# Performance work log

Measured on AMD Instinct MI355X. Metric: run time of the kernel, lower is better.

## Reference

```python
import jax, jax.numpy as jnp
import numpy as np

LAYER_NUM = 2
NUM_CLS = 128
HIDDEN = 256
NUM_NODES = 1024


def setup_inputs() -> dict:
    key = jax.random.key(0)
    ks = jax.random.split(key, 12)
    s = 0.05
    return {
        "x": jax.random.normal(ks[0], (NUM_NODES, HIDDEN), jnp.float32),
        "knowledge": jax.random.uniform(ks[1], (NUM_CLS, NUM_CLS), jnp.float32) / NUM_CLS,
        "w3w": jax.random.normal(ks[2], (HIDDEN, 2 * HIDDEN), jnp.float32) * s,
        "b3w": jax.random.normal(ks[3], (HIDDEN,), jnp.float32) * s,
        "u3": jax.random.normal(ks[4], (HIDDEN, HIDDEN), jnp.float32) * s,
        "bu3": jax.random.normal(ks[5], (HIDDEN,), jnp.float32) * s,
        "w4w": jax.random.normal(ks[6], (HIDDEN, 2 * HIDDEN), jnp.float32) * s,
        "b4w": jax.random.normal(ks[7], (HIDDEN,), jnp.float32) * s,
        "w5w": jax.random.normal(ks[8], (HIDDEN, 2 * HIDDEN), jnp.float32) * s,
        "b5w": jax.random.normal(ks[9], (HIDDEN,), jnp.float32) * s,
        "u5": jax.random.normal(ks[10], (HIDDEN, HIDDEN), jnp.float32) * s,
        "bu5": jax.random.normal(ks[11], (HIDDEN,), jnp.float32) * s,
    }


def reference(x, knowledge, w3w, b3w, u3, bu3, w4w, b4w, w5w, b5w, u5, bu5):
    N, H = x.shape
    C = knowledge.shape[0]
    # hidden[n, c, :] = x[n, :]  (repeat per class)
    hidden = jnp.broadcast_to(x[:, None, :], (N, C, H))
    for _ in range(LAYER_NUM):
        hs = hidden.sum(0)                      # [C, H]
        diff = hs[None, :, :] - hidden          # [N, C, H]
        # knowledge.T @ diff_n  and  knowledge @ diff_n, vectorized over nodes
        left = jnp.einsum('kc,nkh->nch', knowledge, diff)
        right = jnp.einsum('ck,nkh->nch', knowledge, diff)
        av = jnp.concatenate([left, right], axis=-1).reshape(N * C, 2 * H)
        h = hidden.reshape(N * C, H)
        uh3 = h @ u3.T + bu3                    # shared: rv uses fc_eq3_u (source quirk)
        zv = jax.nn.sigmoid(av @ w3w.T + b3w + uh3)
        rv = jax.nn.sigmoid(av @ w4w.T + b4w + uh3)
        hv = jnp.tanh(av @ w5w.T + b5w + (rv * h) @ u5.T + bu5)
        h = (1.0 - zv) * h + zv * hv
        hidden = h.reshape(N, C, H)
    return hidden
```

## Files before the change

### kernel.cpp

```cpp
#include <hip/hip_runtime.h>
#include <cstdint>
#include <cstddef>


#define NODES 1024
#define NCLS  128
#define HID   256

using frag  = __attribute__((ext_vector_type(8))) short;
using frag4 = __attribute__((ext_vector_type(4))) short;
using f32x4 = __attribute__((ext_vector_type(4))) float;

__device__ __forceinline__ float bf2f(unsigned short h){
  unsigned int u = ((unsigned int)h) << 16;
  float f; __builtin_memcpy(&f, &u, 4); return f;
}
__device__ __forceinline__ unsigned short f2bf(float f){
  unsigned int u; __builtin_memcpy(&u, &f, 4);
  u = (u + 0x7fffu + ((u >> 16) & 1u)) >> 16;
  return (unsigned short)u;
}
__device__ __forceinline__ float sigm(float x){ return 1.0f/(1.0f + __expf(-x)); }
__device__ __forceinline__ float tanh_fast(float x){ return 1.0f - 2.0f/(__expf(2.0f*x) + 1.0f); }

#define GLOBAL_AS(p) ((const __attribute__((address_space(1))) void*)(p))
#define LDS_AS(p)    ((__attribute__((address_space(3))) void*)(p))

template<int OUT_BF16>
__global__ __launch_bounds__(256) void gemm_bf16(
    const unsigned short* __restrict__ A0, int ldA0, int K0,
    const unsigned short* __restrict__ A1, int ldA1,
    const unsigned short* __restrict__ BT, int ldB, long bStride,
    void* __restrict__ Cptr, int ldC,
    int Ntiles, int Ktot, unsigned int aMask, int Mtiles)
{
  __shared__ unsigned short As[4096];
  __shared__ unsigned short Bs[4096];
  const int t   = threadIdx.x;
  const int bid = blockIdx.x;
  const int xcd = bid & 7, slot = bid >> 3;
  const int mtPerX = (Mtiles >= 8) ? (Mtiles >> 3) : 1;
  const int mt = xcd * mtPerX + slot / Ntiles;
  const int nt = slot % Ntiles;
  const int lane = t & 63, w = t >> 6;
  const int wm = w >> 1, wn = w & 1;
  const int r = lane & 15, q = lane >> 4;
  const int m0 = mt * 128, n0 = nt * 128;
  const unsigned short* Bbase = BT + (size_t)mt * (size_t)bStride;

  f32x4 acc[4][4] = {};

  for (int kb = 0; kb < Ktot; kb += 32) {
#pragma unroll
    for (int i = 0; i < 2; ++i) {
      int u  = i * 256 + t;
      int mi = u >> 2;
      int kc = (u & 3) * 8;
      int k  = kb + kc;
      const unsigned short* ga;
      if (k < K0) ga = A0 + (size_t)((unsigned int)(m0 + mi) & aMask) * (size_t)ldA0 + k;
      else        ga = A1 + (size_t)(m0 + mi) * (size_t)ldA1 + (k - K0);
      __builtin_amdgcn_global_load_lds(GLOBAL_AS(ga), LDS_AS(&As[u * 8]), 16, 0, 0);
      const unsigned short* gb = Bbase + (size_t)(n0 + mi) * (size_t)ldB + k;
      __builtin_amdgcn_global_load_lds(GLOBAL_AS(gb), LDS_AS(&Bs[u * 8]), 16, 0, 0);
    }
    __syncthreads();

    frag af[4], bf_[4];
#pragma unroll
    for (int x = 0; x < 4; ++x) {
      af[x]  = *(const frag*)&As[(wm * 64 + x * 16 + r) * 32 + q * 8];
      bf_[x] = *(const frag*)&Bs[(wn * 64 + x * 16 + r) * 32 + q * 8];
    }
#pragma unroll
    for (int x = 0; x < 4; ++x)
#pragma unroll
      for (int y = 0; y < 4; ++y)
        acc[x][y] = __builtin_amdgcn_mfma_f32_16x16x32_bf16(af[x], bf_[y], acc[x][y], 0, 0, 0);
    __syncthreads();
  }

#pragma unroll
  for (int x = 0; x < 4; ++x) {
#pragma unroll
    for (int y = 0; y < 4; ++y) {
      int col = n0 + wn * 64 + y * 16 + r;
#pragma unroll
      for (int g = 0; g < 4; ++g) {
        long row = m0 + wm * 64 + x * 16 + q * 4 + g;
        if (OUT_BF16) ((unsigned short*)Cptr)[row * (long)ldC + col] = f2bf(acc[x][y][g]);
        else          ((float*)Cptr)[row * (long)ldC + col] = acc[x][y][g];
      }
    }
  }
}

__global__ __launch_bounds__(512) void gemm_node(
    const unsigned short* __restrict__ KTbN, const unsigned short* __restrict__ KbN,
    const unsigned short* __restrict__ H1T, const unsigned short* __restrict__ H1,
    const unsigned short* __restrict__ WB, unsigned short* __restrict__ PRE)
{
  __shared__ unsigned short Qs[128 * 512];
  __shared__ unsigned short As[2][4096];
  __shared__ unsigned short Bs[2][4096];

  const int t   = threadIdx.x;
  const int bid = blockIdx.x;
  const int node = (bid & 7) * 128 + (bid >> 3);
  const int g  = t >> 8;
  const int tg = t & 255;
  const int w  = t >> 6;
  const int wl = w & 3;
  const int wm = wl >> 1, wn = wl & 1;
  const int lane = t & 63;
  const int r = lane & 15, q = lane >> 4;

  f32x4 acc[4][4];

  const unsigned short* Ksrc = g ? KbN : KTbN;
  for (int hh = 0; hh < 2; ++hh) {
#pragma unroll
    for (int x = 0; x < 4; ++x)
#pragma unroll
      for (int y = 0; y < 4; ++y) acc[x][y] = (f32x4){0.f, 0.f, 0.f, 0.f};

    for (int kb = 0; kb < 128; kb += 32) {
#pragma unroll
      for (int i = 0; i < 2; ++i) {
        int u = i * 256 + tg;
        int mi = u >> 2, kc = (u & 3) * 8;
        __builtin_amdgcn_global_load_lds(GLOBAL_AS(Ksrc + (size_t)mi * 128 + kb + kc),
                                         LDS_AS(&As[g][u * 8]), 16, 0, 0);
      }
      {
        int mi = t >> 2, kc = (t & 3) * 8;
        __builtin_amdgcn_global_load_lds(GLOBAL_AS(H1T + (size_t)node * (HID * NCLS)
                                           + (size_t)(hh * 128 + mi) * 128 + kb + kc),
                                         LDS_AS(&Bs[0][t * 8]), 16, 0, 0);
      }
      __syncthreads();

      frag af[4], bf_[4];
#pragma unroll
      for (int x = 0; x < 4; ++x) {
        af[x]  = *(const frag*)&As[g][(wm * 64 + x * 16 + r) * 32 + q * 8];
        bf_[x] = *(const frag*)&Bs[0][(wn * 64 + x * 16 + r) * 32 + q * 8];
      }
#pragma unroll
      for (int x = 0; x < 4; ++x)
#pragma unroll
        for (int y = 0; y < 4; ++y)
          acc[x][y] = __builtin_amdgcn_mfma_f32_16x16x32_bf16(af[x], bf_[y], acc[x][y], 0, 0, 0);
      __syncthreads();
    }

    int jBase = g * 256 + hh * 128;
#pragma unroll
    for (int x = 0; x < 4; ++x)
#pragma unroll
      for (int y = 0; y < 4; ++y)
#pragma unroll
        for (int gg = 0; gg < 4; ++gg) {
          int c = wm * 64 + x * 16 + q * 4 + gg;
          int j = jBase + wn * 64 + y * 16 + r;
          int jblk = (j >> 3) ^ (c & 7);
          Qs[c * 512 + jblk * 8 + (j & 7)] = f2bf(acc[x][y][gg]);
        }
  }
  __syncthreads();

  for (int rd = 0; rd < 3; ++rd) {
    const int ct = rd * 2 + g;
    const int kmax = (rd < 2) ? 768 : 512;
#pragma unroll
    for (int x = 0; x < 4; ++x)
#pragma unroll
      for (int y = 0; y < 4; ++y) acc[x][y] = (f32x4){0.f, 0.f, 0.f, 0.f};

    for (int kb = 0; kb < kmax; kb += 32) {
#pragma unroll
      for (int i = 0; i < 2; ++i) {
        int u = i * 256 + tg;
        int mi = u >> 2, kc = (u & 3) * 8;
        __builtin_amdgcn_global_load_lds(GLOBAL_AS(WB + (size_t)(ct * 128 + mi) * 768 + kb + kc),
                                         LDS_AS(&Bs[g][u * 8]), 16, 0, 0);
      }
      if (kb >= 512) {
        int mi = t >> 2, kc = (t & 3) * 8;
        __builtin_amdgcn_global_load_lds(GLOBAL_AS(H1 + (size_t)(node * 128 + mi) * 256
                                           + (kb - 512) + kc),
                                         LDS_AS(&As[0][t * 8]), 16, 0, 0);
      }
      __syncthreads();

      frag af[4], bf_[4];
      if (kb < 512) {
        int jb0 = (kb >> 3) + q;
#pragma unroll
        for (int x = 0; x < 4; ++x) {
          int c = wm * 64 + x * 16 + r;
          int jblk = jb0 ^ (c & 7);
          af[x] = *(const frag*)&Qs[c * 512 + jblk * 8];
        }
      } else {
#pragma unroll
        for (int x = 0; x < 4; ++x)
          af[x] = *(const frag*)&As[0][(wm * 64 + x * 16 + r) * 32 + q * 8];
      }
#pragma unroll
      for (int y = 0; y < 4; ++y)
        bf_[y] = *(const frag*)&Bs[g][(wn * 64 + y * 16 + r) * 32 + q * 8];
#pragma unroll
      for (int x = 0; x < 4; ++x)
#pragma unroll
        for (int y = 0; y < 4; ++y)
          acc[x][y] = __builtin_amdgcn_mfma_f32_16x16x32_bf16(af[x], bf_[y], acc[x][y], 0, 0, 0);
      __syncthreads();
    }

#pragma unroll
    for (int x = 0; x < 4; ++x)
#pragma unroll
      for (int y = 0; y < 4; ++y) {
        int lc = wn * 64 + y * 16 + r;
#pragma unroll
        for (int gg = 0; gg < 4; ++gg) {
          int c = wm * 64 + x * 16 + q * 4 + gg;
          PRE[(size_t)(node * 128 + c) * 768 + ct * 128 + lc] = f2bf(acc[x][y][gg]);
        }
      }
  }
}

__global__ __launch_bounds__(256) void gemm_l1(
    const float* __restrict__ XW, const float* __restrict__ SW,
    const float* __restrict__ x,
    const float* __restrict__ b3, const float* __restrict__ b4,
    const float* __restrict__ b5, const float* __restrict__ bu3,
    const float* __restrict__ bu5,
    const float* __restrict__ colsum, const float* __restrict__ rowsum,
    const unsigned short* __restrict__ u5b,
    unsigned short* __restrict__ H1, unsigned short* __restrict__ H1T)
{
  __shared__ unsigned short As[4096], Bs[4096];
  __shared__ float tP1[256], tP2[256], tP3[256], tX[256];
  __shared__ float tZ1[256], tZ2[256], tZ3[256];
  __shared__ float tV1[256], tV2[256], tV3[256];
  __shared__ float tCS[128], tRS[128];

  const int t = threadIdx.x, bid = blockIdx.x;
  const int xcd = bid & 7, slot = bid >> 3;
  const int n  = xcd * 128 + (slot >> 1);
  const int nt = slot & 1;
  const int lane = t & 63, w = t >> 6, wm = w >> 1, wn = w & 1;
  const int r = lane & 15, q = lane >> 4;
  const int n0 = nt * 128;
  const float* xw = XW + (size_t)n * 1792;

  {
    int i = t;
    float xwi0 = xw[i], xwi1 = xw[256 + i], xwi2 = xw[512 + i], xwi3 = xw[768 + i];
    float xwi4 = xw[1024 + i], xwi5 = xw[1280 + i], xwu = xw[1536 + i];
    tP1[i] = SW[512 + i] - xwi2;
    tP2[i] = SW[768 + i] - xwi3;
    tP3[i] = xwu + b4[i] + bu3[i];
    tX[i]  = x[(size_t)n * HID + i];
    tZ1[i] = SW[i] - xwi0;
    tZ2[i] = SW[256 + i] - xwi1;
    tZ3[i] = xwu + b3[i] + bu3[i];
    tV1[i] = SW[1024 + i] - xwi4;
    tV2[i] = SW[1280 + i] - xwi5;
    tV3[i] = b5[i] + bu5[i];
    if (t < 128) { tCS[t] = colsum[t]; tRS[t] = rowsum[t]; }
  }
  __syncthreads();

  f32x4 acc[4][4] = {};

  for (int kb = 0; kb < 256; kb += 32) {
#pragma unroll
    for (int i = 0; i < 2; ++i) {
      int u  = i * 256 + t;
      int mi = u >> 2;
      int kc = (u & 3) * 8;
      int k  = kb + kc;
      __builtin_amdgcn_global_load_lds(GLOBAL_AS(u5b + (size_t)(n0 + mi) * 256 + k),
                                       LDS_AS(&Bs[u * 8]), 16, 0, 0);
      float cs = tCS[mi], rs = tRS[mi];
      frag a;
#pragma unroll
      for (int e = 0; e < 8; ++e) {
        int i2 = k + e;
        float pre = cs * tP1[i2] + rs * tP2[i2] + tP3[i2];
        a[e] = (short)f2bf(sigm(pre) * tX[i2]);
      }
      *(frag*)&As[u * 8] = a;
    }
    __syncthreads();

    frag af[4], bf_[4];
#pragma unroll
    for (int xx = 0; xx < 4; ++xx) {
      af[xx]  = *(const frag*)&As[(wm * 64 + xx * 16 + r) * 32 + q * 8];
      bf_[xx] = *(const frag*)&Bs[(wn * 64 + xx * 16 + r) * 32 + q * 8];
    }
#pragma unroll
    for (int xx = 0; xx < 4; ++xx)
#pragma unroll
      for (int y = 0; y < 4; ++y)
        acc[xx][y] = __builtin_amdgcn_mfma_f32_16x16x32_bf16(af[xx], bf_[y], acc[xx][y], 0, 0, 0);
    __syncthreads();
  }

#pragma unroll
  for (int xx = 0; xx < 4; ++xx) {
#pragma unroll
    for (int y = 0; y < 4; ++y) {
      int i = n0 + wn * 64 + y * 16 + r;
      frag4 pack;
#pragma unroll
      for (int g = 0; g < 4; ++g) {
        int c = wm * 64 + xx * 16 + q * 4 + g;
        float cs = tCS[c], rs = tRS[c];
        float z  = sigm(cs * tZ1[i] + rs * tZ2[i] + tZ3[i]);
        float p5 = cs * tV1[i] + rs * tV2[i] + tV3[i] + acc[xx][y][g];
        float h1 = (1.0f - z) * tX[i] + z * tanh_fast(p5);
        unsigned short hb = f2bf(h1);
        pack[g] = (short)hb;
        H1[(size_t)(n * 128 + c) * HID + i] = hb;
      }
      *(frag4*)(H1T + (size_t)n * (HID * NCLS) + (size_t)i * NCLS
                + (wm * 64 + xx * 16 + q * 4)) = pack;
    }
  }
}

__global__ __launch_bounds__(256) void gemm_l2(
    const unsigned short* __restrict__ PRE, const float* __restrict__ SG,
    const unsigned short* __restrict__ H1, const unsigned short* __restrict__ u5b,
    float* __restrict__ out)
{
  __shared__ unsigned short As[4096], Bs[4096];
  const int t = threadIdx.x, bid = blockIdx.x;
  const int xcd = bid & 7, slot = bid >> 3;
  const int mt = xcd * 128 + (slot >> 1);
  const int nt = slot & 1;
  const int lane = t & 63, w = t >> 6, wm = w >> 1, wn = w & 1;
  const int r = lane & 15, q = lane >> 4;
  const int m0 = mt * 128, n0 = nt * 128;

  f32x4 acc[4][4] = {};

  for (int kb = 0; kb < 256; kb += 32) {
#pragma unroll
    for (int i = 0; i < 2; ++i) {
      int u  = i * 256 + t;
      int mi = u >> 2;
      int kc = (u & 3) * 8;
      int k  = kb + kc;
      __builtin_amdgcn_global_load_lds(GLOBAL_AS(u5b + (size_t)(n0 + mi) * 256 + k),
                                       LDS_AS(&Bs[u * 8]), 16, 0, 0);
      long row = m0 + mi;
      frag p4 = *(const frag*)(PRE + row * 768 + 256 + k);
      frag h1 = *(const frag*)(H1 + row * 256 + k);
      const float* sg = SG + (size_t)mi * 768 + 256 + k;
      frag a;
#pragma unroll
      for (int e = 0; e < 8; ++e) {
        float rv = sigm(sg[e] + bf2f((unsigned short)p4[e]));
        a[e] = (short)f2bf(rv * bf2f((unsigned short)h1[e]));
      }
      *(frag*)&As[u * 8] = a;
    }
    __syncthreads();

    frag af[4], bf_[4];
#pragma unroll
    for (int xx = 0; xx < 4; ++xx) {
      af[xx]  = *(const frag*)&As[(wm * 64 + xx * 16 + r) * 32 + q * 8];
      bf_[xx] = *(const frag*)&Bs[(wn * 64 + xx * 16 + r) * 32 + q * 8];
    }
#pragma unroll
    for (int xx = 0; xx < 4; ++xx)
#pragma unroll
      for (int y = 0; y < 4; ++y)
        acc[xx][y] = __builtin_amdgcn_mfma_f32_16x16x32_bf16(af[xx], bf_[y], acc[xx][y], 0, 0, 0);
    __syncthreads();
  }

#pragma unroll
  for (int xx = 0; xx < 4; ++xx) {
#pragma unroll
    for (int y = 0; y < 4; ++y) {
      int i = n0 + wn * 64 + y * 16 + r;
#pragma unroll
      for (int g = 0; g < 4; ++g) {
        int c = wm * 64 + xx * 16 + q * 4 + g;
        long row = m0 + c;
        float z  = sigm(SG[(size_t)c * 768 + i] + bf2f(PRE[row * 768 + i]));
        float pv = SG[(size_t)c * 768 + 512 + i] + bf2f(PRE[row * 768 + 512 + i])
                 + acc[xx][y][g];
        float h  = bf2f(H1[row * 256 + i]);
        out[row * 256 + i] = (1.0f - z) * h + z * tanh_fast(pv);
      }
    }
  }
}

__global__ __launch_bounds__(256) void prep_cast(
    const float* __restrict__ x, const float* __restrict__ Kn,
    const float* __restrict__ w3, const float* __restrict__ u3,
    const float* __restrict__ w4, const float* __restrict__ w5,
    const float* __restrict__ u5,
    unsigned short* __restrict__ xb, unsigned short* __restrict__ WB,
    unsigned short* __restrict__ WB2, unsigned short* __restrict__ u5b,
    unsigned short* __restrict__ KbN, unsigned short* __restrict__ KTbN)
{
  int idx = blockIdx.x * 256 + threadIdx.x;
  if (idx < 262144) { xb[idx] = f2bf(x[idx]); return; }
  idx -= 262144;
  if (idx < 589824) {
    int col = idx / 768, j = idx % 768;
    int g = col >> 8, i = col & 255;
    float v;
    if (j < 512) { const float* wg = (g == 0) ? w3 : (g == 1) ? w4 : w5; v = wg[(size_t)i * 512 + j]; }
    else v = (g < 2) ? u3[(size_t)i * 256 + (j - 512)] : 0.0f;
    WB[(size_t)col * 768 + j] = f2bf(v);
    return;
  }
  idx -= 589824;
  if (idx < 458752) {
    int col = idx / 256, h = idx % 256;
    int b = col >> 8, i = col & 255;
    float v = (b < 6) ? ((b < 2 ? w3 : (b < 4 ? w4 : w5))[(size_t)i * 512 + (b & 1) * 256 + h])
                      : u3[(size_t)i * 256 + h];
    WB2[(size_t)col * 256 + h] = f2bf(v);
    return;
  }
  idx -= 458752;
  if (idx < 65536) { u5b[idx] = f2bf(u5[idx]); return; }
  idx -= 65536;
  if (idx < 16384) { int c = idx >> 7, k = idx & 127; KbN[idx]  = f2bf(-Kn[c * 128 + k]); return; }
  idx -= 16384;
  { int c = idx >> 7, k = idx & 127; KTbN[idx] = f2bf(-Kn[k * 128 + c]); }
}

__global__ __launch_bounds__(256) void prep_reduce(
    const float* __restrict__ x, const float* __restrict__ Kn,
    float* __restrict__ S, float* __restrict__ colsum, float* __restrict__ rowsum)
{
  int b = blockIdx.x, t = threadIdx.x;
  if (b < 8) {
    float s = 0.f;
    for (int n = 0; n < 128; ++n) s += x[(size_t)(b * 128 + n) * HID + t];
    atomicAdd(&S[t], s);
  } else if (b == 8) {
    if (t < NCLS) { float s = 0.f; for (int k = 0; k < NCLS; ++k) s += Kn[k * NCLS + t]; colsum[t] = s; }
  } else {
    if (t < NCLS) { float s = 0.f; for (int k = 0; k < NCLS; ++k) s += Kn[t * NCLS + k]; rowsum[t] = s; }
  }
}

__global__ __launch_bounds__(256) void prep_sw(
    const float* __restrict__ S, const float* __restrict__ w3,
    const float* __restrict__ w4, const float* __restrict__ w5, float* __restrict__ SW)
{
  int col = blockIdx.x * 256 + threadIdx.x;
  int b = col >> 8, i = col & 255;
  const float* w = (b < 2) ? w3 : (b < 4) ? w4 : w5;
  const float* row = w + (size_t)i * 512 + (b & 1) * 256;
  float s = 0.f;
  for (int h = 0; h < HID; ++h) s += S[h] * row[h];
  SW[col] = s;
}

__global__ __launch_bounds__(256) void reduce_hs(
    const unsigned short* __restrict__ H1, float* __restrict__ hs)
{
  int bid = blockIdx.x;
  int c = bid >> 5, nch = bid & 31;
  int i = threadIdx.x;
  const unsigned short* p = H1 + (size_t)nch * 32 * NCLS * HID + (size_t)c * HID + i;
  float s = 0.f;
  for (int n = 0; n < 32; ++n) s += bf2f(p[(size_t)n * NCLS * HID]);
  atomicAdd(&hs[c * HID + i], s);
}

__global__ __launch_bounds__(256) void p2a(
    const float* __restrict__ hs, const float* __restrict__ w3,
    const float* __restrict__ w4, const float* __restrict__ w5, float* __restrict__ hsW)
{
  __shared__ float hrow[HID];
  int k = blockIdx.x & 127, b = blockIdx.x >> 7;
  int t = threadIdx.x;
  hrow[t] = hs[k * HID + t];
  __syncthreads();
  const float* w = (b < 2) ? w3 : (b < 4) ? w4 : w5;
  const float* row = w + (size_t)t * 512 + (b & 1) * 256;
  float s = 0.f;
  for (int h = 0; h < HID; ++h) s += hrow[h] * row[h];
  hsW[(size_t)k * 1536 + b * 256 + t] = s;
}

__global__ __launch_bounds__(256) void p2b(
    const float* __restrict__ hsW, const float* __restrict__ Kn,
    const float* __restrict__ b3, const float* __restrict__ b4, const float* __restrict__ b5,
    const float* __restrict__ bu3, const float* __restrict__ bu5, float* __restrict__ SG)
{
  __shared__ float kc[NCLS], kr[NCLS];
  int c = blockIdx.x, t = threadIdx.x;
  if (t < NCLS) { kc[t] = Kn[t * NCLS + c]; kr[t] = Kn[c * NCLS + t]; }
  __syncthreads();
  for (int g = 0; g < 3; ++g) {
    int i = t;
    const float* L = hsW + (size_t)(2 * g) * 256 + i;
    const float* R = hsW + (size_t)(2 * g + 1) * 256 + i;
    float s = 0.f;
    for (int k = 0; k < NCLS; ++k) s += kc[k] * L[(size_t)k * 1536] + kr[k] * R[(size_t)k * 1536];
    const float* bg = (g == 0) ? b3 : (g == 1) ? b4 : b5;
    s += bg[i] + ((g < 2) ? bu3[i] : bu5[i]);
    SG[(size_t)c * 768 + g * 256 + i] = s;
  }
}

extern "C" void kernel_launch(void* const* d_in, const int* in_sizes, int n_in,
                              void* d_out, int out_size, void* d_ws, size_t ws_size,
                              hipStream_t stream) {
  (void)in_sizes; (void)n_in; (void)out_size; (void)ws_size;
  const float* x   = (const float*)d_in[0];
  const float* Kn  = (const float*)d_in[1];
  const float* w3  = (const float*)d_in[2];
  const float* b3  = (const float*)d_in[3];
  const float* u3  = (const float*)d_in[4];
  const float* bu3 = (const float*)d_in[5];
  const float* w4  = (const float*)d_in[6];
  const float* b4  = (const float*)d_in[7];
  const float* w5  = (const float*)d_in[8];
  const float* b5  = (const float*)d_in[9];
  const float* u5  = (const float*)d_in[10];
  const float* bu5 = (const float*)d_in[11];
  float* out = (float*)d_out;

  char* w = (char*)d_ws;
  unsigned short* PRE = (unsigned short*)(w);
  unsigned short* H1  = (unsigned short*)(w + 201326592);
  unsigned short* H1T = (unsigned short*)(w + 268435456);
  float*          XW  = (float*)(w + 335544320);
  char* misc = w + 342884352;
  float* S      = (float*)(misc);
  float* hs     = (float*)(misc + 1024);
  float* SW     = (float*)(misc + 132096);
  float* colsum = (float*)(misc + 138240);
  float* rowsum = (float*)(misc + 138752);
  float* hsW    = (float*)(misc + 139264);
  float* SG     = (float*)(misc + 925696);
  unsigned short* WB   = (unsigned short*)(misc + 1318912);
  unsigned short* WB2  = (unsigned short*)(misc + 2498560);
  unsigned short* u5b  = (unsigned short*)(misc + 3416064);
  unsigned short* KbN  = (unsigned short*)(misc + 3547136);
  unsigned short* KTbN = (unsigned short*)(misc + 3579904);
  unsigned short* xb   = (unsigned short*)(misc + 3612672);

  hipMemsetAsync(misc, 0, 132096, stream);

  prep_cast<<<5504, 256, 0, stream>>>(x, Kn, w3, u3, w4, w5, u5, xb, WB, WB2, u5b, KbN, KTbN);
  prep_reduce<<<10, 256, 0, stream>>>(x, Kn, S, colsum, rowsum);
  prep_sw<<<6, 256, 0, stream>>>(S, w3, w4, w5, SW);

  gemm_bf16<0><<<8 * 14, 256, 0, stream>>>(xb, 256, 256, xb, 256, WB2, 256, 0L,
                                           (void*)XW, 1792, 14, 256, 0xFFFFFFFFu, 8);
  gemm_l1<<<2048, 256, 0, stream>>>(XW, SW, x, b3, b4, b5, bu3, bu5,
                                    colsum, rowsum, u5b, H1, H1T);

  reduce_hs<<<4096, 256, 0, stream>>>(H1, hs);
  p2a<<<768, 256, 0, stream>>>(hs, w3, w4, w5, hsW);
  p2b<<<128, 256, 0, stream>>>(hsW, Kn, b3, b4, b5, bu3, bu5, SG);

  gemm_node<<<1024, 512, 0, stream>>>(KTbN, KbN, H1T, H1, WB, PRE);

  gemm_l2<<<2048, 256, 0, stream>>>(PRE, SG, H1, u5b, out);
}
```

Before: 836.7 us.

## Split fused per-node GEMM into separate AV and PRE kernels via global buffer

Replaces the single 512-thread gemm_node kernel, which kept the per-node AV product in a 128KB LDS buffer, with two 256-thread kernels. The first computes the knowledge-times-hidden products into a new 128MB global AVH buffer. The second multiplies AVH (plus H1) by the packed weights to produce PRE. The aim is to lift the occupancy limit imposed by the large LDS footprint and get smaller, more schedulable blocks. The cost is an extra round-trip of the intermediate through global memory and additional kernel launches.

```diff
diff --git a/kernel.cpp b/kernel.cpp
--- a/kernel.cpp
+++ b/kernel.cpp
@@ -95,140 +95,152 @@
   }
 }
 
-__global__ __launch_bounds__(512) void gemm_node(
-    const unsigned short* __restrict__ KTbN, const unsigned short* __restrict__ KbN,
-    const unsigned short* __restrict__ H1T, const unsigned short* __restrict__ H1,
-    const unsigned short* __restrict__ WB, unsigned short* __restrict__ PRE)
-{
-  __shared__ unsigned short Qs[128 * 512];
-  __shared__ unsigned short As[2][4096];
-  __shared__ unsigned short Bs[2][4096];
-
+__global__ __launch_bounds__(256, 4) void gemm_avh(
+    const unsigned short* __restrict__ Ksrc, const unsigned short* __restrict__ H1T,
+    unsigned short* __restrict__ AVH, int colOff)
+{
+  __shared__ unsigned short As[4096];
+  __shared__ unsigned short Bs[4096];
   const int t   = threadIdx.x;
   const int bid = blockIdx.x;
-  const int node = (bid & 7) * 128 + (bid >> 3);
-  const int g  = t >> 8;
-  const int tg = t & 255;
-  const int w  = t >> 6;
-  const int wl = w & 3;
-  const int wm = wl >> 1, wn = wl & 1;
-  const int lane = t & 63;
+  const int xcd = bid & 7, slot = bid >> 3;
+  const int node = xcd * 128 + (slot >> 1);
+  const int nt = slot & 1;
+  const int lane = t & 63, w = t >> 6;
+  const int wm = w >> 1, wn = w & 1;
   const int r = lane & 15, q = lane >> 4;
-
-  f32x4 acc[4][4];
-
-  const unsigned short* Ksrc = g ? KbN : KTbN;
-  for (int hh = 0; hh < 2; ++hh) {
+  const int n0 = nt * 128;
+  const unsigned short* Bbase = H1T + (size_t)node * (HID * NCLS);
+
+  f32x4 acc[4][4] = {};
+
+  for (int kb = 0; kb < 128; kb += 32) {
+#pragma unroll
+    for (int i = 0; i < 2; ++i) {
+      int u  = i * 256 + t;
+      int mi = u >> 2;
+      int kc = (u & 3) * 8;
+      __builtin_amdgcn_global_load_lds(GLOBAL_AS(Ksrc + (size_t)mi * 128 + kb + kc),
+                                       LDS_AS(&As[u * 8]), 16, 0, 0);
+      __builtin_amdgcn_global_load_lds(GLOBAL_AS(Bbase + (size_t)(n0 + mi) * 128 + kb + kc),
+                                       LDS_AS(&Bs[u * 8]), 16, 0, 0);
+    }
+    __syncthreads();
+
+    frag af[4], bf_[4];
+#pragma unroll
+    for (int x = 0; x < 4; ++x) {
+      af[x]  = *(const frag*)&As[(wm * 64 + x * 16 + r) * 32 + q * 8];
+      bf_[x] = *(const frag*)&Bs[(wn * 64 + x * 16 + r) * 32 + q * 8];
+    }
 #pragma unroll
     for (int x = 0; x < 4; ++x)
 #pragma unroll
-      for (int y = 0; y < 4; ++y) acc[x][y] = (f32x4){0.f, 0.f, 0.f, 0.f};
-
-    for (int kb = 0; kb < 128; kb += 32) {
-#pragma unroll
-      for (int i = 0; i < 2; ++i) {
-        int u = i * 256 + tg;
-        int mi = u >> 2, kc = (u & 3) * 8;
-        __builtin_amdgcn_global_load_lds(GLOBAL_AS(Ksrc + (size_t)mi * 128 + kb + kc),
-                                         LDS_AS(&As[g][u * 8]), 16, 0, 0);
-      }
-      {
-        int mi = t >> 2, kc = (t & 3) * 8;
-        __builtin_amdgcn_global_load_lds(GLOBAL_AS(H1T + (size_t)node * (HID * NCLS)
-                                           + (size_t)(hh * 128 + mi) * 128 + kb + kc),
-                                         LDS_AS(&Bs[0][t * 8]), 16, 0, 0);
-      }
-      __syncthreads();
-
-      frag af[4], bf_[4];
-#pragma unroll
-      for (int x = 0; x < 4; ++x) {
-        af[x]  = *(const frag*)&As[g][(wm * 64 + x * 16 + r) * 32 + q * 8];
-        bf_[x] = *(const frag*)&Bs[0][(wn * 64 + x * 16 + r) * 32 + q * 8];
-      }
-#pragma unroll
-      for (int x = 0; x < 4; ++x)
-#pragma unroll
-        for (int y = 0; y < 4; ++y)
-          acc[x][y] = __builtin_amdgcn_mfma_f32_16x16x32_bf16(af[x], bf_[y], acc[x][y], 0, 0, 0);
-      __syncthreads();
-    }
-
-    int jBase = g * 256 + hh * 128;
+      for (int y = 0; y < 4; ++y)
+        acc[x][y] = __builtin_amdgcn_mfma_f32_16x16x32_bf16(af[x], bf_[y], acc[x][y], 0, 0, 0);
+    __syncthreads();
+  }
+
+#pragma unroll
+  for (int x = 0; x < 4; ++x) {
+#pragma unroll
+    for (int y = 0; y < 4; ++y) {
+      int col = colOff + n0 + wn * 64 + y * 16 + r;
+#pragma unroll
+      for (int g = 0; g < 4; ++g) {
+        long row = (long)node * 128 + wm * 64 + x * 16 + q * 4 + g;
+        AVH[row * 512 + col] = f2bf(acc[x][y][g]);
+      }
+    }
+  }
+}
+
+__global__ __launch_bounds__(256, 4) void gemm_pre(
+    const unsigned short* __restrict__ AVH, const unsigned short* __restrict__ H1,
+    const unsigned short* __restrict__ WB, unsigned short* __restrict__ PRE,
+    int ctBase, int Ntiles, int Ktot)
+{
+  __shared__ unsigned short As[4096];
+  __shared__ unsigned short Bs[4096];
+  const int t   = threadIdx.x;
+  const int bid = blockIdx.x;
+  const int xcd = bid & 7, slot = bid >> 3;
+  const int mt = xcd * 128 + slot / Ntiles;
+  const int ct = ctBase + slot % Ntiles;
+  const int lane = t & 63, w = t >> 6;
+  const int wm = w >> 1, wn = w & 1;
+  const int r = lane & 15, q = lane >> 4;
+  const int m0 = mt * 128;
+  const int mi = (2 * 256 + 0, t >> 2) ;
+  (void)mi;
+
+  f32x4 acc[4][4] = {};
+
+  for (int kb = 0; kb < 512; kb += 32) {
+#pragma unroll
+    for (int i = 0; i < 2; ++i) {
+      int u  = i * 256 + t;
+      int m  = u >> 2;
+      int kc = (u & 3) * 8;
+      __builtin_amdgcn_global_load_lds(GLOBAL_AS(AVH + (size_t)(m0 + m) * 512 + kb + kc),
+                                       LDS_AS(&As[u * 8]), 16, 0, 0);
+      __builtin_amdgcn_global_load_lds(GLOBAL_AS(WB + (size_t)(ct * 128 + m) * 768 + kb + kc),
+                                       LDS_AS(&Bs[u * 8]), 16, 0, 0);
+    }
+    __syncthreads();
+
+    frag af[4], bf_[4];
+#pragma unroll
+    for (int x = 0; x < 4; ++x) {
+      af[x]  = *(const frag*)&As[(wm * 64 + x * 16 + r) * 32 + q * 8];
+      bf_[x] = *(const frag*)&Bs[(wn * 64 + x * 16 + r) * 32 + q * 8];
+    }
 #pragma unroll
     for (int x = 0; x < 4; ++x)
 #pragma unroll
       for (int y = 0; y < 4; ++y)
-#pragma unroll
-        for (int gg = 0; gg < 4; ++gg) {
-          int c = wm * 64 + x * 16 + q * 4 + gg;
-          int j = jBase + wn * 64 + y * 16 + r;
-          int jblk = (j >> 3) ^ (c & 7);
-          Qs[c * 512 + jblk * 8 + (j & 7)] = f2bf(acc[x][y][gg]);
-        }
-  }
-  __syncthreads();
-
-  for (int rd = 0; rd < 3; ++rd) {
-    const int ct = rd * 2 + g;
-    const int kmax = (rd < 2) ? 768 : 512;
+        acc[x][y] = __builtin_amdgcn_mfma_f32_16x16x32_bf16(af[x], bf_[y], acc[x][y], 0, 0, 0);
+    __syncthreads();
+  }
+
+  for (int kb = 512; kb < Ktot; kb += 32) {
+#pragma unroll
+    for (int i = 0; i < 2; ++i) {
+      int u  = i * 256 + t;
+      int m  = u >> 2;
+      int kc = (u & 3) * 8;
+      __builtin_amdgcn_global_load_lds(GLOBAL_AS(H1 + (size_t)(m0 + m) * 256 + (kb - 512) + kc),
+                                       LDS_AS(&As[u * 8]), 16, 0, 0);
+      __builtin_amdgcn_global_load_lds(GLOBAL_AS(WB + (size_t)(ct * 128 + m) * 768 + kb + kc),
+                                       LDS_AS(&Bs[u * 8]), 16, 0, 0);
+    }
+    __syncthreads();
+
+    frag af[4], bf_[4];
+#pragma unroll
+    for (int x = 0; x < 4; ++x) {
+      af[x]  = *(const frag*)&As[(wm * 64 + x * 16 + r) * 32 + q * 8];
+      bf_[x] = *(const frag*)&Bs[(wn * 64 + x * 16 + r) * 32 + q * 8];
+    }
 #pragma unroll
     for (int x = 0; x < 4; ++x)
 #pragma unroll
-      for (int y = 0; y < 4; ++y) acc[x][y] = (f32x4){0.f, 0.f, 0.f, 0.f};
-
-    for (int kb = 0; kb < kmax; kb += 32) {
-#pragma unroll
-      for (int i = 0; i < 2; ++i) {
-        int u = i * 256 + tg;
-        int mi = u >> 2, kc = (u & 3) * 8;
-        __builtin_amdgcn_global_load_lds(GLOBAL_AS(WB + (size_t)(ct * 128 + mi) * 768 + kb + kc),
-                                         LDS_AS(&Bs[g][u * 8]), 16, 0, 0);
-      }
-      if (kb >= 512) {
-        int mi = t >> 2, kc = (t & 3) * 8;
-        __builtin_amdgcn_global_load_lds(GLOBAL_AS(H1 + (size_t)(node * 128 + mi) * 256
-                                           + (kb - 512) + kc),
-                                         LDS_AS(&As[0][t * 8]), 16, 0, 0);
-      }
-      __syncthreads();
-
-      frag af[4], bf_[4];
-      if (kb < 512) {
-        int jb0 = (kb >> 3) + q;
-#pragma unroll
-        for (int x = 0; x < 4; ++x) {
-          int c = wm * 64 + x * 16 + r;
-          int jblk = jb0 ^ (c & 7);
-          af[x] = *(const frag*)&Qs[c * 512 + jblk * 8];
-        }
-      } else {
-#pragma unroll
-        for (int x = 0; x < 4; ++x)
-          af[x] = *(const frag*)&As[0][(wm * 64 + x * 16 + r) * 32 + q * 8];
-      }
-#pragma unroll
       for (int y = 0; y < 4; ++y)
-        bf_[y] = *(const frag*)&Bs[g][(wn * 64 + y * 16 + r) * 32 + q * 8];
-#pragma unroll
-      for (int x = 0; x < 4; ++x)
-#pragma unroll
-        for (int y = 0; y < 4; ++y)
-          acc[x][y] = __builtin_amdgcn_mfma_f32_16x16x32_bf16(af[x], bf_[y], acc[x][y], 0, 0, 0);
-      __syncthreads();
-    }
-
-#pragma unroll
-    for (int x = 0; x < 4; ++x)
-#pragma unroll
-      for (int y = 0; y < 4; ++y) {
-        int lc = wn * 64 + y * 16 + r;
-#pragma unroll
-        for (int gg = 0; gg < 4; ++gg) {
-          int c = wm * 64 + x * 16 + q * 4 + gg;
-          PRE[(size_t)(node * 128 + c) * 768 + ct * 128 + lc] = f2bf(acc[x][y][gg]);
-        }
-      }
+        acc[x][y] = __builtin_amdgcn_mfma_f32_16x16x32_bf16(af[x], bf_[y], acc[x][y], 0, 0, 0);
+    __syncthreads();
+  }
+
+#pragma unroll
+  for (int x = 0; x < 4; ++x) {
+#pragma unroll
+    for (int y = 0; y < 4; ++y) {
+      int col = ct * 128 + wn * 64 + y * 16 + r;
+#pragma unroll
+      for (int g = 0; g < 4; ++g) {
+        long row = m0 + wm * 64 + x * 16 + q * 4 + g;
+        PRE[row * 768 + col] = f2bf(acc[x][y][g]);
+      }
+    }
   }
 }
 
@@ -542,11 +554,12 @@
   float* out = (float*)d_out;
 
   char* w = (char*)d_ws;
-  unsigned short* PRE = (unsigned short*)(w);
-  unsigned short* H1  = (unsigned short*)(w + 201326592);
-  unsigned short* H1T = (unsigned short*)(w + 268435456);
-  float*          XW  = (float*)(w + 335544320);
-  char* misc = w + 342884352;
+  unsigned short* AVH = (unsigned short*)(w);
+  unsigned short* PRE = (unsigned short*)(w + 134217728);
+  unsigned short* H1  = (unsigned short*)(w + 335544320);
+  unsigned short* H1T = (unsigned short*)(w + 402653184);
+  float*          XW  = (float*)(w + 469762048);
+  char* misc = w + 477102080;
   float* S      = (float*)(misc);
   float* hs     = (float*)(misc + 1024);
   float* SW     = (float*)(misc + 132096);
@@ -576,7 +589,11 @@
   p2a<<<768, 256, 0, stream>>>(hs, w3, w4, w5, hsW);
   p2b<<<128, 256, 0, stream>>>(hsW, Kn, b3, b4, b5, bu3, bu5, SG);
 
-  gemm_node<<<1024, 512, 0, stream>>>(KTbN, KbN, H1T, H1, WB, PRE);
+  gemm_avh<<<2048, 256, 0, stream>>>(KTbN, H1T, AVH, 0);
+  gemm_avh<<<2048, 256, 0, stream>>>(KbN, H1T, AVH, 256);
+
+  gemm_pre<<<1024 * 4, 256, 0, stream>>>(AVH, H1, WB, PRE, 0, 4, 768);
+  gemm_pre<<<1024 * 2, 256, 0, stream>>>(AVH, H1, WB, PRE, 4, 2, 512);
 
   gemm_l2<<<2048, 256, 0, stream>>>(PRE, SG, H1, u5b, out);
 }
```

Result: no change. 829.9 us (-0.8%).
